# Performance work log

Measured on AMD Instinct MI355X. Metric: run time of the kernel, lower is better.

## Reference

```python
import jax, jax.numpy as jnp
import numpy as np

D_MODEL, D_STATE, EXPAND = 1024, 256, 2
BATCH, SEQ = 8, 2048


def setup_inputs() -> dict:
    key = jax.random.key(0)
    ks = jax.random.split(key, 7)
    s = 0.02
    return {
        "x": jax.random.normal(ks[0], (BATCH, SEQ, D_MODEL), jnp.float32),
        "W_in": jax.random.normal(ks[1], (D_MODEL, D_MODEL * EXPAND), jnp.float32) * s,
        "b_in": jax.random.normal(ks[2], (D_MODEL * EXPAND,), jnp.float32) * s,
        "W_state": jax.random.normal(ks[3], (D_MODEL * EXPAND, D_STATE), jnp.float32) * s,
        "b_state": jax.random.normal(ks[4], (D_STATE,), jnp.float32) * s,
        "W_out": jax.random.normal(ks[5], (D_STATE, D_MODEL), jnp.float32) * s,
        "b_out": jax.random.normal(ks[6], (D_MODEL,), jnp.float32) * s,
        "init_state": jnp.zeros((1, D_STATE), jnp.float32),
    }


def reference(x, W_in, b_in, W_state, b_state, W_out, b_out, init_state):
    # x: [B, T, D]
    x_proj = jax.nn.silu(jnp.einsum("btd,de->bte", x, W_in) + b_in)  # [B,T,2D]
    # state_proj depends only on x_proj, so batch the GEMM over all timesteps
    updates = jnp.einsum("bte,es->bts", x_proj, W_state) + b_state    # [B,T,S]
    updates_t = jnp.swapaxes(updates, 0, 1)                            # [T,B,S]
    state0 = jnp.broadcast_to(init_state, (x.shape[0], init_state.shape[1]))

    def step(state, u):
        new = jax.nn.silu(state + u)
        return new, new

    _, states = jax.lax.scan(step, state0, updates_t)  # [T,B,S]
    out = jnp.einsum("tbs,sd->tbd", states, W_out) + b_out  # [T,B,D]
    return jnp.swapaxes(out, 0, 1)  # [B,T,D]
```

## Files before the change

### kernel.cpp

```cpp
#include <hip/hip_runtime.h>
#include <cstdint>
#include <cstddef>

#define BATCH 8
#define SEQ   2048
#define DM    1024
#define DE    2048
#define DSZ   256
#define MROWS (BATCH*SEQ)
#define MCHUNK 8192

typedef _Float16 f16;
typedef _Float16 f16x4 __attribute__((ext_vector_type(4)));
typedef _Float16 f16x8 __attribute__((ext_vector_type(8)));
typedef float  f32x4  __attribute__((ext_vector_type(4)));

__device__ __forceinline__ void glds16(const void* gp, void* lp) {
  __builtin_amdgcn_global_load_lds(
      (const __attribute__((address_space(1))) void*)gp,
      (__attribute__((address_space(3))) void*)lp, 16, 0, 0);
}

__device__ __forceinline__ float silu_f(float x) {
  return x * __builtin_amdgcn_rcpf(1.0f + __expf(-x));
}

__global__ void split_x_k(const float* __restrict__ in, f16* __restrict__ oh,
                          f16* __restrict__ ol, int n) {
  int i = (blockIdx.x * blockDim.x + threadIdx.x) * 4;
  const int stride = gridDim.x * blockDim.x * 4;
  for (; i < n; i += stride) {
    float4 v = *(const float4*)(in + i);
    f16x4 h, l;
    h[0] = (f16)v.x; l[0] = (f16)(v.x - (float)h[0]);
    h[1] = (f16)v.y; l[1] = (f16)(v.y - (float)h[1]);
    h[2] = (f16)v.z; l[2] = (f16)(v.z - (float)h[2]);
    h[3] = (f16)v.w; l[3] = (f16)(v.w - (float)h[3]);
    *(f16x4*)(oh + i) = h;
    *(f16x4*)(ol + i) = l;
  }
}

__global__ void transpose_split_k(const float* __restrict__ in, f16* __restrict__ oh,
                                  f16* __restrict__ ol, int R, int C) {
  __shared__ float tile[32][33];
  const int c0 = blockIdx.x * 32, r0 = blockIdx.y * 32;
  const int tx = threadIdx.x, ty = threadIdx.y;
  #pragma unroll
  for (int i = 0; i < 4; ++i)
    tile[ty + i*8][tx] = in[(size_t)(r0 + ty + i*8) * C + c0 + tx];
  __syncthreads();
  #pragma unroll
  for (int i = 0; i < 4; ++i) {
    float v = tile[tx][ty + i*8];
    f16 h = (f16)v;
    size_t idx = (size_t)(c0 + ty + i*8) * R + r0 + tx;
    oh[idx] = h;
    ol[idx] = (f16)(v - (float)h);
  }
}

__global__ void transpose_cast_f16_k(const float* __restrict__ in, f16* __restrict__ out, int R, int C) {
  __shared__ float tile[32][33];
  const int c0 = blockIdx.x * 32, r0 = blockIdx.y * 32;
  const int tx = threadIdx.x, ty = threadIdx.y;
  #pragma unroll
  for (int i = 0; i < 4; ++i)
    tile[ty + i*8][tx] = in[(size_t)(r0 + ty + i*8) * C + c0 + tx];
  __syncthreads();
  #pragma unroll
  for (int i = 0; i < 4; ++i)
    out[(size_t)(c0 + ty + i*8) * R + r0 + tx] = (f16)tile[tx][ty + i*8];
}

__global__ __launch_bounds__(512) void gemm1_k(const f16* __restrict__ Ah, const f16* __restrict__ Al,
                                               const f16* __restrict__ Bh, const f16* __restrict__ Bl,
                                               const float* __restrict__ bias,
                                               f16* __restrict__ Ch, f16* __restrict__ Cl) {
  const int K = 1024, N = 2048;
  __shared__ f16 sAh[4096], sAl[4096], sBh[4096], sBl[4096];

  const int tid = threadIdx.x;
  const int w = tid >> 6, l = tid & 63;
  const int bm = blockIdx.y * 128, bn = blockIdx.x * 128;
  const int wm = (w >> 2) * 64, wn = (w & 3) * 32;
  const int lr = l & 15, lq = l >> 4;

  const int r = tid >> 2, k8 = tid & 3;
  const f16* pAh = Ah + (size_t)(bm + r) * K + k8 * 8;
  const f16* pAl = Al + (size_t)(bm + r) * K + k8 * 8;
  const f16* pBh = Bh + (size_t)(bn + r) * K + k8 * 8;
  const f16* pBl = Bl + (size_t)(bn + r) * K + k8 * 8;
  f16* dAh = sAh + tid * 8; f16* dAl = sAl + tid * 8;
  f16* dBh = sBh + tid * 8; f16* dBl = sBl + tid * 8;

  int offA[4], offB[2];
  #pragma unroll
  for (int i = 0; i < 4; ++i) offA[i] = (wm + i*16 + lr) * 32 + lq * 8;
  #pragma unroll
  for (int j = 0; j < 2; ++j) offB[j] = (wn + j*16 + lr) * 32 + lq * 8;

  f32x4 acc[4][2] = {};

  for (int kk = 0; kk < K; kk += 32) {
    __syncthreads();
    glds16(pAh, dAh); glds16(pAl, dAl);
    glds16(pBh, dBh); glds16(pBl, dBl);
    pAh += 32; pAl += 32; pBh += 32; pBl += 32;
    asm volatile("s_waitcnt vmcnt(0)" ::: "memory");
    __syncthreads();

    f16x8 ah[4], al[4], bh[2], bl[2];
    #pragma unroll
    for (int i = 0; i < 4; ++i) {
      ah[i] = *(const f16x8*)(sAh + offA[i]);
      al[i] = *(const f16x8*)(sAl + offA[i]);
    }
    #pragma unroll
    for (int j = 0; j < 2; ++j) {
      bh[j] = *(const f16x8*)(sBh + offB[j]);
      bl[j] = *(const f16x8*)(sBl + offB[j]);
    }
    #pragma unroll
    for (int i = 0; i < 4; ++i)
      #pragma unroll
      for (int j = 0; j < 2; ++j) {
        acc[i][j] = __builtin_amdgcn_mfma_f32_16x16x32_f16(ah[i], bh[j], acc[i][j], 0, 0, 0);
        acc[i][j] = __builtin_amdgcn_mfma_f32_16x16x32_f16(ah[i], bl[j], acc[i][j], 0, 0, 0);
        acc[i][j] = __builtin_amdgcn_mfma_f32_16x16x32_f16(al[i], bh[j], acc[i][j], 0, 0, 0);
      }
  }

  #pragma unroll
  for (int j = 0; j < 2; ++j) {
    const int col = bn + wn + j*16 + lr;
    const float bv = bias[col];
    #pragma unroll
    for (int i = 0; i < 4; ++i)
      #pragma unroll
      for (int r4 = 0; r4 < 4; ++r4) {
        const int row = bm + wm + i*16 + lq*4 + r4;
        const float s = silu_f(acc[i][j][r4] + bv);
        const f16 h = (f16)s;
        const size_t idx = (size_t)row * N + col;
        Ch[idx] = h;
        Cl[idx] = (f16)(s - (float)h);
      }
  }
}

__global__ __launch_bounds__(256) void gemm2s_k(const f16* __restrict__ Ah, const f16* __restrict__ Al,
                                                const f16* __restrict__ Bh, const f16* __restrict__ Bl,
                                                const float* __restrict__ bias,
                                                float* __restrict__ C) {
  const int K = 2048, N = 256;
  __shared__ f16 sAh[2048], sAl[2048], sBh[4096], sBl[4096];

  const int tid = threadIdx.x;
  const int w = tid >> 6, l = tid & 63;
  const int bm = blockIdx.y * 64, bn = blockIdx.x * 128;
  const int wm = (w & 1) * 32, wn = (w >> 1) * 64;
  const int lr = l & 15, lq = l >> 4;

  const int rA = tid >> 2, k8 = tid & 3;
  const f16* pAh = Ah + (size_t)(bm + rA) * K + k8 * 8;
  const f16* pAl = Al + (size_t)(bm + rA) * K + k8 * 8;
  f16* dAh = sAh + tid * 8; f16* dAl = sAl + tid * 8;
  const f16 *pBh[2], *pBl[2]; f16 *dBh[2], *dBl[2];
  #pragma unroll
  for (int p = 0; p < 2; ++p) {
    const int c = p * 256 + tid;
    const int rB = c >> 2;
    pBh[p] = Bh + (size_t)(bn + rB) * K + (c & 3) * 8;
    pBl[p] = Bl + (size_t)(bn + rB) * K + (c & 3) * 8;
    dBh[p] = sBh + (size_t)c * 8; dBl[p] = sBl + (size_t)c * 8;
  }

  int offA[2], offB[4];
  #pragma unroll
  for (int i = 0; i < 2; ++i) offA[i] = (wm + i*16 + lr) * 32 + lq * 8;
  #pragma unroll
  for (int j = 0; j < 4; ++j) offB[j] = (wn + j*16 + lr) * 32 + lq * 8;

  f32x4 acc[2][4] = {};

  for (int kk = 0; kk < K; kk += 32) {
    __syncthreads();
    glds16(pAh, dAh); glds16(pAl, dAl);
    pAh += 32; pAl += 32;
    #pragma unroll
    for (int p = 0; p < 2; ++p) {
      glds16(pBh[p], dBh[p]); pBh[p] += 32;
      glds16(pBl[p], dBl[p]); pBl[p] += 32;
    }
    asm volatile("s_waitcnt vmcnt(0)" ::: "memory");
    __syncthreads();

    f16x8 ah[2], al[2], bh[4], bl[4];
    #pragma unroll
    for (int i = 0; i < 2; ++i) {
      ah[i] = *(const f16x8*)(sAh + offA[i]);
      al[i] = *(const f16x8*)(sAl + offA[i]);
    }
    #pragma unroll
    for (int j = 0; j < 4; ++j) {
      bh[j] = *(const f16x8*)(sBh + offB[j]);
      bl[j] = *(const f16x8*)(sBl + offB[j]);
    }
    #pragma unroll
    for (int i = 0; i < 2; ++i)
      #pragma unroll
      for (int j = 0; j < 4; ++j) {
        acc[i][j] = __builtin_amdgcn_mfma_f32_16x16x32_f16(ah[i], bh[j], acc[i][j], 0, 0, 0);
        acc[i][j] = __builtin_amdgcn_mfma_f32_16x16x32_f16(ah[i], bl[j], acc[i][j], 0, 0, 0);
        acc[i][j] = __builtin_amdgcn_mfma_f32_16x16x32_f16(al[i], bh[j], acc[i][j], 0, 0, 0);
      }
  }

  #pragma unroll
  for (int j = 0; j < 4; ++j) {
    const int col = bn + wn + j*16 + lr;
    const float bv = bias[col];
    #pragma unroll
    for (int i = 0; i < 2; ++i)
      #pragma unroll
      for (int r4 = 0; r4 < 4; ++r4) {
        const int row = bm + wm + i*16 + lq*4 + r4;
        C[(size_t)row * N + col] = acc[i][j][r4] + bv;
      }
  }
}

__global__ __launch_bounds__(256) void gemm3_k(const f16* __restrict__ A,
                                               const f16* __restrict__ Bt,
                                               const float* __restrict__ bias,
                                               float* __restrict__ C) {
  const int K = 256, N = 1024;
  __shared__ f16 sA[4096], sB[4096];

  const int tid = threadIdx.x;
  const int w = tid >> 6, l = tid & 63;
  const int bm = blockIdx.y * 128, bn = blockIdx.x * 128;
  const int wm = (w >> 1) * 64, wn = (w & 1) * 64;
  const int lr = l & 15, lq = l >> 4;

  const f16 *pA[2], *pB[2]; f16 *dA[2], *dB[2];
  #pragma unroll
  for (int p = 0; p < 2; ++p) {
    const int c = p * 256 + tid;
    const int r = c >> 2, k8 = c & 3;
    pA[p] = A  + (size_t)(bm + r) * K + k8 * 8;
    pB[p] = Bt + (size_t)(bn + r) * K + k8 * 8;
    dA[p] = sA + (size_t)c * 8;
    dB[p] = sB + (size_t)c * 8;
  }

  int offA[4], offB[4];
  #pragma unroll
  for (int i = 0; i < 4; ++i) {
    offA[i] = (wm + i*16 + lr) * 32 + lq * 8;
    offB[i] = (wn + i*16 + lr) * 32 + lq * 8;
  }

  f32x4 acc[4][4] = {};

  for (int kk = 0; kk < K; kk += 32) {
    __syncthreads();
    glds16(pA[0], dA[0]); glds16(pA[1], dA[1]);
    glds16(pB[0], dB[0]); glds16(pB[1], dB[1]);
    pA[0] += 32; pA[1] += 32; pB[0] += 32; pB[1] += 32;
    asm volatile("s_waitcnt vmcnt(0)" ::: "memory");
    __syncthreads();

    f16x8 af[4], bfr[4];
    #pragma unroll
    for (int i = 0; i < 4; ++i) af[i]  = *(const f16x8*)(sA + offA[i]);
    #pragma unroll
    for (int j = 0; j < 4; ++j) bfr[j] = *(const f16x8*)(sB + offB[j]);
    #pragma unroll
    for (int i = 0; i < 4; ++i)
      #pragma unroll
      for (int j = 0; j < 4; ++j)
        acc[i][j] = __builtin_amdgcn_mfma_f32_16x16x32_f16(af[i], bfr[j], acc[i][j], 0, 0, 0);
  }

  #pragma unroll
  for (int j = 0; j < 4; ++j) {
    const int col = bn + wn + j*16 + lr;
    const float bv = bias[col];
    #pragma unroll
    for (int i = 0; i < 4; ++i)
      #pragma unroll
      for (int r4 = 0; r4 < 4; ++r4) {
        const int row = bm + wm + i*16 + lq*4 + r4;
        C[(size_t)row * N + col] = acc[i][j][r4] + bv;
      }
  }
}

__global__ void scan_k(const float* __restrict__ upd, const float* __restrict__ init,
                       f16* __restrict__ states) {
  const int b = blockIdx.x, s = threadIdx.x;
  const float* u = upd + (size_t)b * SEQ * DSZ + s;
  f16* st = states + (size_t)b * SEQ * DSZ + s;
  float state = init[s];
  float ubuf[16];
  #pragma unroll
  for (int i = 0; i < 16; ++i) ubuf[i] = u[(size_t)i * DSZ];
  for (int t0 = 0; t0 < SEQ; t0 += 16) {
    #pragma unroll
    for (int i = 0; i < 16; ++i) {
      const int t = t0 + i;
      const float x = state + ubuf[i];
      state = silu_f(x);
      st[(size_t)t * DSZ] = (f16)state;
      const int tn = t + 16;
      ubuf[i] = (tn < SEQ) ? u[(size_t)tn * DSZ] : 0.0f;
    }
  }
}

extern "C" void kernel_launch(void* const* d_in, const int* in_sizes, int n_in,
                              void* d_out, int out_size, void* d_ws, size_t ws_size,
                              hipStream_t stream) {
  const float* x       = (const float*)d_in[0];
  const float* W_in    = (const float*)d_in[1];
  const float* b_in    = (const float*)d_in[2];
  const float* W_state = (const float*)d_in[3];
  const float* b_state = (const float*)d_in[4];
  const float* W_out   = (const float*)d_in[5];
  const float* b_out   = (const float*)d_in[6];
  const float* init_st = (const float*)d_in[7];
  float* out = (float*)d_out;

  char* ws = (char*)d_ws;
  f16*   xh        = (f16*)(ws + 0);
  f16*   xl        = (f16*)(ws + 33554432);
  f16*   xproj_h   = (f16*)(ws + 67108864);
  f16*   xproj_l   = (f16*)(ws + 100663296);
  float* upd       = (float*)(ws + 134217728);
  f16*   states    = (f16*)(ws + 150994944);
  f16*   w_in_h    = (f16*)(ws + 159383552);
  f16*   w_in_l    = (f16*)(ws + 163577856);
  f16*   w_state_h = (f16*)(ws + 167772160);
  f16*   w_state_l = (f16*)(ws + 168820736);
  f16*   w_out_t   = (f16*)(ws + 169869312);

  split_x_k<<<4096, 256, 0, stream>>>(x, xh, xl, MROWS * DM);
  dim3 tb(32, 8);
  transpose_split_k<<<dim3(DE/32,  DM/32), tb, 0, stream>>>(W_in,    w_in_h,    w_in_l,    DM,  DE);
  transpose_split_k<<<dim3(DSZ/32, DE/32), tb, 0, stream>>>(W_state, w_state_h, w_state_l, DE,  DSZ);
  transpose_cast_f16_k<<<dim3(DM/32, DSZ/32), tb, 0, stream>>>(W_out, w_out_t, DSZ, DM);

  for (int c = 0; c < 2; ++c) {
    const size_t ro = (size_t)c * MCHUNK;
    gemm1_k<<<dim3(DE/128, MCHUNK/128), 512, 0, stream>>>(
        xh + ro * DM, xl + ro * DM, w_in_h, w_in_l, b_in, xproj_h, xproj_l);
    gemm2s_k<<<dim3(DSZ/128, MCHUNK/64), 256, 0, stream>>>(
        xproj_h, xproj_l, w_state_h, w_state_l, b_state, upd + ro * DSZ);
  }

  scan_k<<<BATCH, DSZ, 0, stream>>>(upd, init_st, states);

  gemm3_k<<<dim3(DM/128, MROWS/128), 256, 0, stream>>>(states, w_out_t, b_out, out);
}
```

Before: 633.2 us.

## Remap gemm1 tiles per XCD and shorten scan critical path with prefetch

gemm1 now runs on a 1D grid and remaps block IDs so that consecutive blocks dispatched to the same XCD cover neighbouring M tiles. This is meant to improve L2 reuse of the A and B tiles within each XCD. The scan kernel double-buffers the update loads one 16-step chunk ahead and precomputes u*(-log2e), so each step's exp2 argument is a single FMA off the serial dependency chain. Stores are batched after each chunk, which costs extra registers.

Result: no change. 625.4 us (-1.2%).

```diff
diff --git a/kernel.cpp b/kernel.cpp
--- a/kernel.cpp
+++ b/kernel.cpp
@@ -82,7 +82,11 @@
 
   const int tid = threadIdx.x;
   const int w = tid >> 6, l = tid & 63;
-  const int bm = blockIdx.y * 128, bn = blockIdx.x * 128;
+  const int bid = blockIdx.x;
+  const int xcd = bid & 7, loc = bid >> 3;
+  const int mt = xcd * 8 + (loc & 7);
+  const int nt = loc >> 3;
+  const int bm = mt * 128, bn = nt * 128;
   const int wm = (w >> 2) * 64, wn = (w & 3) * 32;
   const int lr = l & 15, lq = l >> 4;
 
@@ -298,25 +302,37 @@
   }
 }
 
+#define L2E 1.4426950408889634f
 __global__ void scan_k(const float* __restrict__ upd, const float* __restrict__ init,
                        f16* __restrict__ states) {
   const int b = blockIdx.x, s = threadIdx.x;
   const float* u = upd + (size_t)b * SEQ * DSZ + s;
   f16* st = states + (size_t)b * SEQ * DSZ + s;
   float state = init[s];
-  float ubuf[16];
-  #pragma unroll
-  for (int i = 0; i < 16; ++i) ubuf[i] = u[(size_t)i * DSZ];
+
+  float ucur[16], unext[16], ulog[16];
+  #pragma unroll
+  for (int i = 0; i < 16; ++i) ucur[i] = u[(size_t)i * DSZ];
+  #pragma unroll
+  for (int i = 0; i < 16; ++i) ulog[i] = ucur[i] * (-L2E);
+
   for (int t0 = 0; t0 < SEQ; t0 += 16) {
+    if (t0 + 16 < SEQ) {
+      #pragma unroll
+      for (int i = 0; i < 16; ++i) unext[i] = u[(size_t)(t0 + 16 + i) * DSZ];
+    }
+    f16 res[16];
     #pragma unroll
     for (int i = 0; i < 16; ++i) {
-      const int t = t0 + i;
-      const float x = state + ubuf[i];
-      state = silu_f(x);
-      st[(size_t)t * DSZ] = (f16)state;
-      const int tn = t + 16;
-      ubuf[i] = (tn < SEQ) ? u[(size_t)tn * DSZ] : 0.0f;
-    }
+      const float e = __builtin_amdgcn_exp2f(__builtin_fmaf(state, -L2E, ulog[i]));
+      const float x = state + ucur[i];
+      state = x * __builtin_amdgcn_rcpf(1.0f + e);
+      res[i] = (f16)state;
+    }
+    #pragma unroll
+    for (int i = 0; i < 16; ++i) st[(size_t)(t0 + i) * DSZ] = res[i];
+    #pragma unroll
+    for (int i = 0; i < 16; ++i) { ucur[i] = unext[i]; ulog[i] = unext[i] * (-L2E); }
   }
 }
 
@@ -354,7 +370,7 @@
 
   for (int c = 0; c < 2; ++c) {
     const size_t ro = (size_t)c * MCHUNK;
-    gemm1_k<<<dim3(DE/128, MCHUNK/128), 512, 0, stream>>>(
+    gemm1_k<<<1024, 512, 0, stream>>>(
         xh + ro * DM, xl + ro * DM, w_in_h, w_in_l, b_in, xproj_h, xproj_l);
     gemm2s_k<<<dim3(DSZ/128, MCHUNK/64), 256, 0, stream>>>(
         xproj_h, xproj_l, w_state_h, w_state_l, b_state, upd + ro * DSZ);
```
